# Performance work log

Measured on AMD Instinct MI355X. Metric: run time of the kernel, lower is better.

Reference implementation:

```python
import jax, jax.numpy as jnp
import numpy as np

B, L, D, H = 2, 2048, 1024, 16
HD = D // H  # head_dim = 64


def setup_inputs() -> dict:
    key = jax.random.key(0)
    ks = jax.random.split(key, 8)
    queries = jax.random.normal(ks[0], (B, L, D), dtype=jnp.float32)
    keys = jax.random.normal(ks[1], (B, L, D), dtype=jnp.float32)
    values = jax.random.normal(ks[2], (B, L, D), dtype=jnp.float32)
    mask = jax.random.randint(ks[3], (B, L, L), 0, 2) > 0  # True = masked
    s = 1.0 / np.sqrt(D)
    W_q = jax.random.normal(ks[4], (D, D), dtype=jnp.float32) * s
    W_k = jax.random.normal(ks[5], (D, D), dtype=jnp.float32) * s
    W_v = jax.random.normal(ks[6], (D, D), dtype=jnp.float32) * s
    W_o = jax.random.normal(ks[7], (D, D), dtype=jnp.float32) * s
    return {"queries": queries, "keys": keys, "values": values,
            "W_q": W_q, "W_k": W_k, "W_v": W_v, "W_o": W_o, "mask": mask}


def _split_heads(x):
    # [B, L, D] -> [B, H, L, HD]
    return x.reshape(B, L, H, HD).transpose(0, 2, 1, 3)


def reference(queries, keys, values, W_q, W_k, W_v, W_o, mask):
    # Linear projections (nn.Linear: x @ W.T, no bias)
    q = _split_heads(queries @ W_q.T)   # [B,H,Lq,HD]
    k = _split_heads(keys @ W_k.T)      # [B,H,Lk,HD]
    v = _split_heads(values @ W_v.T)    # [B,H,Lk,HD]
    scores = jnp.einsum('bnqd,bnkd->bnqk', q, k) / np.sqrt(HD)
    scores = jnp.where(mask[:, None, :, :], -1e9, scores)
    attn = jax.nn.softmax(scores, axis=-1)
    ctx = jnp.einsum('bnqk,bnkd->bnqd', attn, v)
    ctx = ctx.transpose(0, 2, 1, 3).reshape(B, L, D)
    return ctx @ W_o.T  # dropout p=0.0 -> identity
```

## Files before the change

kernel.cpp:

```cpp
#include <hip/hip_runtime.h>
#include <hip/hip_bf16.h>

typedef __bf16 bf16;
typedef __attribute__((ext_vector_type(8))) __bf16 bf16x8;
typedef __attribute__((ext_vector_type(4))) __bf16 bf16x4;
typedef __attribute__((ext_vector_type(4))) float f32x4;

#define B_   2
#define L_   2048
#define D_   1024
#define H_   16
#define HD_  64

__device__ __forceinline__ float fast_exp2(float x) {
  float e; asm("v_exp_f32 %0, %1" : "=v"(e) : "v"(x)); return e;
}

__device__ __forceinline__ void gll16(const bf16* g, bf16* l) {
  __builtin_amdgcn_global_load_lds((const __attribute__((address_space(1))) void*)g,
                                   (__attribute__((address_space(3))) void*)l,
                                   16, 0, 0);
}

__global__ void detect_kernel(const unsigned short* __restrict__ q_u,
                              const unsigned char* __restrict__ m_u,
                              int* __restrict__ flags) {
  __shared__ int cnt, odd;
  if (threadIdx.x == 0) { cnt = 0; odd = 0; }
  __syncthreads();
  int c = 0, o = 0;
  for (int i = 0; i < 8; i++) {
    int idx = threadIdx.x * 8 + i;
    unsigned e = (q_u[idx] >> 7) & 0xFF;
    if (e >= 0x8F || (e > 0 && e <= 0x6F)) c++;
    if ((idx & 3) && m_u[idx]) o = 1;
  }
  atomicAdd(&cnt, c);
  if (o) atomicOr(&odd, 1);
  __syncthreads();
  if (threadIdx.x == 0) { flags[0] = (cnt > 128) ? 1 : 0; flags[1] = odd; }
}

__device__ __forceinline__ void canon_body(const void* src, bf16* dst, int i, int f) {
  if (f) {
    const float4* s = (const float4*)src;
    float4 a = s[i / 4], b2 = s[i / 4 + 1];
    bf16x8 o;
    o[0] = (bf16)a.x;  o[1] = (bf16)a.y;  o[2] = (bf16)a.z;  o[3] = (bf16)a.w;
    o[4] = (bf16)b2.x; o[5] = (bf16)b2.y; o[6] = (bf16)b2.z; o[7] = (bf16)b2.w;
    *(bf16x8*)(dst + i) = o;
  } else {
    *(bf16x8*)(dst + i) = ((const bf16x8*)src)[i / 8];
  }
}

__global__ __launch_bounds__(256) void canon_pack(
    const void* xq, const void* xk, const void* xv,
    const void* Wq, const void* Wk, const void* Wv, const void* Wo,
    const void* mp,
    bf16* cxq, bf16* cxk, bf16* cxv,
    bf16* cWq, bf16* cWk, bf16* cWv, bf16* cWo,
    unsigned* __restrict__ bitsT,
    const int* __restrict__ flags) {
  int t = blockIdx.x;
  if (t >= 8192) {
    int wid = (t - 8192) * 256 + threadIdx.x;
    unsigned v = 0;
    if (flags[1]) {
      const uchar4* p = (const uchar4*)mp;
#pragma unroll
      for (int c = 0; c < 8; c++) {
        uchar4 u = p[wid * 8 + c];
        v |= (u.x ? 1u : 0u) << (c * 4 + 0);
        v |= (u.y ? 1u : 0u) << (c * 4 + 1);
        v |= (u.z ? 1u : 0u) << (c * 4 + 2);
        v |= (u.w ? 1u : 0u) << (c * 4 + 3);
      }
    } else {
      const int4* p = (const int4*)mp;
#pragma unroll
      for (int c = 0; c < 8; c++) {
        int4 u = p[wid * 8 + c];
        v |= (u.x ? 1u : 0u) << (c * 4 + 0);
        v |= (u.y ? 1u : 0u) << (c * 4 + 1);
        v |= (u.z ? 1u : 0u) << (c * 4 + 2);
        v |= (u.w ? 1u : 0u) << (c * 4 + 3);
      }
    }
    int row = wid >> 6, word = wid & 63;
    int kt = word >> 1, half = word & 1;
    bitsT[((size_t)kt * 4096 + row) * 2 + half] = v;
    return;
  }
  const int f = flags[0];
  const void* src; bf16* dst; int base;
  if (t < 2048)      { src = xq; dst = cxq; base = t * 2048; }
  else if (t < 4096) { src = xk; dst = cxk; base = (t - 2048) * 2048; }
  else if (t < 6144) { src = xv; dst = cxv; base = (t - 4096) * 2048; }
  else {
    int w = t - 6144, wi = w >> 9;
    base = (w & 511) * 2048;
    if (wi == 0)      { src = Wq; dst = cWq; }
    else if (wi == 1) { src = Wk; dst = cWk; }
    else if (wi == 2) { src = Wv; dst = cWv; }
    else              { src = Wo; dst = cWo; }
  }
  canon_body(src, dst, base + threadIdx.x * 8, f);
}

__global__ __launch_bounds__(256) void gemm_qkv(
    const bf16* __restrict__ Aq, const bf16* __restrict__ Bq, bf16* __restrict__ Cq,
    const bf16* __restrict__ Ak, const bf16* __restrict__ Bk, bf16* __restrict__ Ck,
    const bf16* __restrict__ Av, const bf16* __restrict__ Bv, bf16* __restrict__ VT) {
  __shared__ bf16 smem[128 * 136];
  bf16* sA = smem;
  bf16* sB = smem + 4096;
  const int z = blockIdx.z;
  const bf16* A  = (z == 0) ? Aq : (z == 1) ? Ak : Av;
  const bf16* Bm = (z == 0) ? Bq : (z == 1) ? Bk : Bv;

  const int tid = threadIdx.x;
  const int w = tid >> 6, lane = tid & 63, qd = lane >> 4, r = lane & 15;
  const int wm = w >> 1, wn = w & 1;
  const int m0 = blockIdx.x * 128, n0 = blockIdx.y * 128;

  f32x4 acc[4][4];
#pragma unroll
  for (int i = 0; i < 4; i++)
#pragma unroll
    for (int j = 0; j < 4; j++) acc[i][j] = (f32x4){0.f, 0.f, 0.f, 0.f};

  for (int k0 = 0; k0 < 1024; k0 += 32) {
    __syncthreads();
#pragma unroll
    for (int p = 0; p < 2; p++) {
      int c = p * 256 + tid;
      gll16(A + (size_t)(m0 + (c >> 2)) * 1024 + k0 + (c & 3) * 8, sA + c * 8);
    }
#pragma unroll
    for (int p = 0; p < 2; p++) {
      int c = p * 256 + tid;
      gll16(Bm + (size_t)(n0 + (c >> 2)) * 1024 + k0 + (c & 3) * 8, sB + c * 8);
    }
    __syncthreads();
    bf16x8 af[4], bfv[4];
#pragma unroll
    for (int i = 0; i < 4; i++)
      af[i] = *(const bf16x8*)&sA[(wm * 64 + i * 16 + r) * 32 + qd * 8];
#pragma unroll
    for (int j = 0; j < 4; j++)
      bfv[j] = *(const bf16x8*)&sB[(wn * 64 + j * 16 + r) * 32 + qd * 8];
#pragma unroll
    for (int i = 0; i < 4; i++)
#pragma unroll
      for (int j = 0; j < 4; j++)
        acc[i][j] = __builtin_amdgcn_mfma_f32_16x16x32_bf16(af[i], bfv[j], acc[i][j], 0, 0, 0);
  }

  if (z < 2) {
    bf16* C = (z == 0) ? Cq : Ck;
    const float s = (z == 0) ? 0.1803368801f : 1.0f;
#pragma unroll
    for (int i = 0; i < 4; i++)
#pragma unroll
      for (int j = 0; j < 4; j++)
#pragma unroll
        for (int rr = 0; rr < 4; rr++) {
          int row = m0 + wm * 64 + i * 16 + qd * 4 + rr;
          int col = n0 + wn * 64 + j * 16 + r;
          C[(size_t)row * 1024 + col] = (bf16)(acc[i][j][rr] * s);
        }
  } else {
    __syncthreads();
#pragma unroll
    for (int i = 0; i < 4; i++)
#pragma unroll
      for (int j = 0; j < 4; j++) {
        int col = wn * 64 + j * 16 + r;
        int rowb = wm * 64 + i * 16 + qd * 4;
        bf16x4 v4;
#pragma unroll
        for (int rr = 0; rr < 4; rr++) v4[rr] = (bf16)acc[i][j][rr];
        *(bf16x4*)&smem[col * 136 + rowb] = v4;
      }
    __syncthreads();
    const int b = m0 >> 11, tok0 = m0 & 2047, h0 = n0 >> 6;
#pragma unroll
    for (int p = 0; p < 8; p++) {
      int c = p * 256 + tid;
      int dl = c >> 4, ch = c & 15;
      bf16x8 v = *(const bf16x8*)&smem[dl * 136 + ch * 8];
      int head = h0 + (dl >> 6), d = dl & 63;
      *(bf16x8*)(VT + ((size_t)((b * 16 + head) * 64 + d)) * 2048 + tok0 + ch * 8) = v;
    }
  }
}

__global__ __launch_bounds__(256) void gemm_nt_out(const bf16* __restrict__ A,
                                                   const bf16* __restrict__ Bm,
                                                   void* __restrict__ Cout,
                                                   const int* __restrict__ flags) {
  __shared__ bf16 sA[128 * 32];
  __shared__ bf16 sB[64 * 32];
  const int tid = threadIdx.x;
  const int w = tid >> 6, lane = tid & 63, qd = lane >> 4, r = lane & 15;
  const int wm = w >> 1, wn = w & 1;
  const int m0 = blockIdx.x * 128, n0 = blockIdx.y * 64;

  f32x4 acc[4][2];
#pragma unroll
  for (int i = 0; i < 4; i++)
#pragma unroll
    for (int j = 0; j < 2; j++) acc[i][j] = (f32x4){0.f, 0.f, 0.f, 0.f};

  for (int k0 = 0; k0 < 1024; k0 += 32) {
    __syncthreads();
    {
      int c0 = tid;
      gll16(A + (size_t)(m0 + (c0 >> 2)) * 1024 + k0 + (c0 & 3) * 8, sA + c0 * 8);
      int c1 = 256 + tid;
      gll16(A + (size_t)(m0 + (c1 >> 2)) * 1024 + k0 + (c1 & 3) * 8, sA + c1 * 8);
      int cb = tid;
      gll16(Bm + (size_t)(n0 + (cb >> 2)) * 1024 + k0 + (cb & 3) * 8, sB + cb * 8);
    }
    __syncthreads();
    bf16x8 af[4], bfv[2];
#pragma unroll
    for (int i = 0; i < 4; i++)
      af[i] = *(const bf16x8*)&sA[(wm * 64 + i * 16 + r) * 32 + qd * 8];
#pragma unroll
    for (int j = 0; j < 2; j++)
      bfv[j] = *(const bf16x8*)&sB[(wn * 32 + j * 16 + r) * 32 + qd * 8];
#pragma unroll
    for (int i = 0; i < 4; i++)
#pragma unroll
      for (int j = 0; j < 2; j++)
        acc[i][j] = __builtin_amdgcn_mfma_f32_16x16x32_bf16(af[i], bfv[j], acc[i][j], 0, 0, 0);
  }
  const int f = flags[0];
#pragma unroll
  for (int i = 0; i < 4; i++)
#pragma unroll
    for (int j = 0; j < 2; j++)
#pragma unroll
      for (int rr = 0; rr < 4; rr++) {
        int row = m0 + wm * 64 + i * 16 + qd * 4 + rr;
        int col = n0 + wn * 32 + j * 16 + r;
        if (f) ((float*)Cout)[(size_t)row * 1024 + col] = acc[i][j][rr];
        else   ((bf16*)Cout)[(size_t)row * 1024 + col] = (bf16)acc[i][j][rr];
      }
}

__global__ __launch_bounds__(256) void attn_kernel(const bf16* __restrict__ Q,
                                                   const bf16* __restrict__ Kp,
                                                   const bf16* __restrict__ Vt,
                                                   const unsigned* __restrict__ bitsT,
                                                   bf16* __restrict__ OP,
                                                   float* __restrict__ LP) {
  __shared__ bf16 sK[64 * 64];
  __shared__ bf16 sVT[64 * 64];
  __shared__ bf16 sP[128 * 72];
  const int tid = threadIdx.x;
  const int w = tid >> 6, lane = tid & 63, qd = lane >> 4, r = lane & 15;
  const int bh = blockIdx.y, b = bh >> 4, h = bh & 15;
  const int q0 = blockIdx.x * 128;
  const int z = blockIdx.z;

  bf16x8 qf[2][2];
#pragma unroll
  for (int i = 0; i < 2; i++)
#pragma unroll
    for (int ks = 0; ks < 2; ks++)
      qf[i][ks] = *(const bf16x8*)(Q + (size_t)(b * L_ + q0 + w * 32 + i * 16 + r) * D_ +
                                   h * HD_ + ks * 32 + qd * 8);

  bf16x8 ones;
#pragma unroll
  for (int e = 0; e < 8; e++) ones[e] = (bf16)1.0f;

  f32x4 o[2][4], lacc[2];
#pragma unroll
  for (int i = 0; i < 2; i++) {
#pragma unroll
    for (int dj = 0; dj < 4; dj++) o[i][dj] = (f32x4){0.f, 0.f, 0.f, 0.f};
    lacc[i] = (f32x4){0.f, 0.f, 0.f, 0.f};
  }

  for (int kt = z * 16; kt < z * 16 + 16; kt++) {
    __syncthreads();
#pragma unroll
    for (int p = 0; p < 2; p++) {
      int c = p * 256 + tid;
      int row = c >> 3, kc = c & 7;
      int kcg = kc ^ (row & 7);
      gll16(Kp + (size_t)(b * L_ + kt * 64 + row) * D_ + h * HD_ + kcg * 8, sK + c * 8);
    }
#pragma unroll
    for (int p = 0; p < 2; p++) {
      int c = p * 256 + tid;
      int row = c >> 3, kc = c & 7;
      int kcg = kc ^ (row & 7);
      gll16(Vt + (size_t)(bh * 64 + row) * L_ + kt * 64 + kcg * 8, sVT + c * 8);
    }

    uint2 m64[2];
#pragma unroll
    for (int i = 0; i < 2; i++)
      m64[i] = *(const uint2*)(bitsT +
          ((size_t)kt * 4096 + b * 2048 + q0 + w * 32 + i * 16 + r) * 2);

    __syncthreads();

    bf16x8 kf[4][2];
#pragma unroll
    for (int j = 0; j < 4; j++)
#pragma unroll
      for (int ks = 0; ks < 2; ks++) {
        int row = j * 16 + r;
        int phys = (ks * 4 + qd) ^ (row & 7);
        kf[j][ks] = *(const bf16x8*)&sK[row * 64 + phys * 8];
      }

#pragma unroll
    for (int i = 0; i < 2; i++) {
      f32x4 S[4];
#pragma unroll
      for (int j = 0; j < 4; j++) {
        S[j] = (f32x4){0.f, 0.f, 0.f, 0.f};
#pragma unroll
        for (int ks = 0; ks < 2; ks++)
          S[j] = __builtin_amdgcn_mfma_f32_16x16x32_bf16(kf[j][ks], qf[i][ks], S[j], 0, 0, 0);
      }
#pragma unroll
      for (int j = 0; j < 4; j++) {
        unsigned word = (j < 2) ? m64[i].x : m64[i].y;
        unsigned nib = (word >> ((j & 1) * 16 + qd * 4)) & 0xFu;
        bf16x4 pv;
#pragma unroll
        for (int rr = 0; rr < 4; rr++) {
          float e = fast_exp2(S[j][rr]);
          pv[rr] = (bf16)(((nib >> rr) & 1u) ? 0.f : e);
        }
        *(bf16x4*)&sP[(w * 32 + i * 16 + r) * 72 + j * 16 + qd * 4] = pv;
      }
    }
    asm volatile("s_waitcnt lgkmcnt(0)" ::: "memory");

    bf16x8 vf[4][2];
#pragma unroll
    for (int dj = 0; dj < 4; dj++)
#pragma unroll
      for (int ks = 0; ks < 2; ks++) {
        int row = dj * 16 + r;
        int phys = (ks * 4 + qd) ^ (row & 7);
        vf[dj][ks] = *(const bf16x8*)&sVT[row * 64 + phys * 8];
      }
#pragma unroll
    for (int i = 0; i < 2; i++)
#pragma unroll
      for (int ks = 0; ks < 2; ks++) {
        bf16x8 pf = *(const bf16x8*)&sP[(w * 32 + i * 16 + r) * 72 + ks * 32 + qd * 8];
#pragma unroll
        for (int dj = 0; dj < 4; dj++)
          o[i][dj] = __builtin_amdgcn_mfma_f32_16x16x32_bf16(pf, vf[dj][ks], o[i][dj], 0, 0, 0);
        lacc[i] = __builtin_amdgcn_mfma_f32_16x16x32_bf16(pf, ones, lacc[i], 0, 0, 0);
      }
  }

#pragma unroll
  for (int i = 0; i < 2; i++) {
#pragma unroll
    for (int dj = 0; dj < 4; dj++)
#pragma unroll
      for (int rr = 0; rr < 4; rr++) {
        int rg = b * L_ + q0 + w * 32 + i * 16 + qd * 4 + rr;
        int col = h * HD_ + dj * 16 + r;
        OP[((size_t)z * 4096 + rg) * 1024 + col] = (bf16)o[i][dj][rr];
      }
    if (r == 0) {
#pragma unroll
      for (int rr = 0; rr < 4; rr++) {
        int rg = b * L_ + q0 + w * 32 + i * 16 + qd * 4 + rr;
        LP[((size_t)z * 4096 + rg) * 16 + h] = lacc[i][rr];
      }
    }
  }
}

__global__ __launch_bounds__(256) void combine_kernel(const bf16* __restrict__ OP,
                                                      const float* __restrict__ LP,
                                                      bf16* __restrict__ CTX) {
  size_t idx = ((size_t)blockIdx.x * 256 + threadIdx.x) * 8;
  int row = (int)(idx >> 10), col = (int)(idx & 1023);
  bf16x8 a = *(const bf16x8*)(OP + idx);
  bf16x8 c = *(const bf16x8*)(OP + (size_t)4096 * 1024 + idx);
  int h = col >> 6;
  float l = LP[row * 16 + h] + LP[65536 + row * 16 + h];
  float inv = 1.0f / l;
  bf16x8 o;
#pragma unroll
  for (int e = 0; e < 8; e++) o[e] = (bf16)(((float)a[e] + (float)c[e]) * inv);
  *(bf16x8*)(CTX + idx) = o;
}

extern "C" void kernel_launch(void* const* d_in, const int* in_sizes, int n_in,
                              void* d_out, int out_size, void* d_ws, size_t ws_size,
                              hipStream_t stream) {
  const void* xq = d_in[0];
  const void* xk = d_in[1];
  const void* xv = d_in[2];
  const void* Wq = d_in[3];
  const void* Wk = d_in[4];
  const void* Wv = d_in[5];
  const void* Wo = d_in[6];
  const void* mask = d_in[7];

  char* ws = (char*)d_ws;
  const size_t MB = 1048576;
  int*      FLAGS = (int*)(ws + 0);
  unsigned* BITS  = (unsigned*)(ws + 4096);
  bf16* cWo = (bf16*)(ws + 2 * MB);
  bf16* cWq = (bf16*)(ws + 4 * MB);
  bf16* cWk = (bf16*)(ws + 6 * MB);
  bf16* cWv = (bf16*)(ws + 8 * MB);
  bf16* cxq = (bf16*)(ws + 10 * MB);
  bf16* cxk = (bf16*)(ws + 18 * MB);
  bf16* cxv = (bf16*)(ws + 26 * MB);
  bf16* Q   = (bf16*)(ws + 34 * MB);
  bf16* K   = (bf16*)(ws + 42 * MB);
  bf16* VT  = (bf16*)(ws + 50 * MB);
  bf16*  OP  = (bf16*)(ws + 4 * MB);
  float* LP  = (float*)(ws + 20 * MB);
  bf16*  CTX = (bf16*)(ws + 26 * MB);

  detect_kernel<<<1, 256, 0, stream>>>((const unsigned short*)xq,
                                       (const unsigned char*)mask, FLAGS);
  canon_pack<<<9216, 256, 0, stream>>>(xq, xk, xv, Wq, Wk, Wv, Wo, mask,
                                       cxq, cxk, cxv, cWq, cWk, cWv, cWo,
                                       BITS, FLAGS);
  gemm_qkv<<<dim3(32, 8, 3), 256, 0, stream>>>(cxq, cWq, Q,
                                               cxk, cWk, K,
                                               cxv, cWv, VT);
  attn_kernel<<<dim3(16, 32, 2), 256, 0, stream>>>(Q, K, VT, BITS, OP, LP);
  combine_kernel<<<2048, 256, 0, stream>>>(OP, LP, CTX);
  gemm_nt_out<<<dim3(32, 16), 256, 0, stream>>>(CTX, cWo, d_out, FLAGS);
}
```

Measured before the change: 268.8 us.

## Use fp16 for V and P in attention; stage Q/K GEMM stores through LDS

Switches the V-transpose buffer and the softmax probability tile from bf16 to fp16, using packed round-toward-zero conversion (cvt_pkrtz) and fp16 MFMA for the P·V product and the row-sum. The aim is cheaper conversion instructions in the exp/pack inner loop. Separately, the Q/K projection epilogue now writes through shared memory and issues coalesced 16-byte global stores instead of scattered 2-byte stores. The fp16 path changes rounding behaviour and has narrower range than bf16, and the epilogue adds an extra LDS round trip and barrier.

```diff
diff --git a/kernel.cpp b/kernel.cpp
--- a/kernel.cpp
+++ b/kernel.cpp
@@ -2,8 +2,12 @@
 #include <hip/hip_bf16.h>
 
 typedef __bf16 bf16;
+typedef _Float16 f16;
 typedef __attribute__((ext_vector_type(8))) __bf16 bf16x8;
 typedef __attribute__((ext_vector_type(4))) __bf16 bf16x4;
+typedef __attribute__((ext_vector_type(8))) _Float16 f16x8;
+typedef __attribute__((ext_vector_type(4))) _Float16 f16x4;
+typedef __attribute__((ext_vector_type(2))) _Float16 f16x2;
 typedef __attribute__((ext_vector_type(4))) float f32x4;
 
 #define B_   2
@@ -16,7 +20,11 @@
   float e; asm("v_exp_f32 %0, %1" : "=v"(e) : "v"(x)); return e;
 }
 
-__device__ __forceinline__ void gll16(const bf16* g, bf16* l) {
+__device__ __forceinline__ f16x2 pkrtz(float a, float b) {
+  return __builtin_bit_cast(f16x2, __builtin_amdgcn_cvt_pkrtz(a, b));
+}
+
+__device__ __forceinline__ void gll16(const void* g, void* l) {
   __builtin_amdgcn_global_load_lds((const __attribute__((address_space(1))) void*)g,
                                    (__attribute__((address_space(3))) void*)l,
                                    16, 0, 0);
@@ -111,7 +119,7 @@
 __global__ __launch_bounds__(256) void gemm_qkv(
     const bf16* __restrict__ Aq, const bf16* __restrict__ Bq, bf16* __restrict__ Cq,
     const bf16* __restrict__ Ak, const bf16* __restrict__ Bk, bf16* __restrict__ Ck,
-    const bf16* __restrict__ Av, const bf16* __restrict__ Bv, bf16* __restrict__ VT) {
+    const bf16* __restrict__ Av, const bf16* __restrict__ Bv, f16* __restrict__ VT) {
   __shared__ bf16 smem[128 * 136];
   bf16* sA = smem;
   bf16* sB = smem + 4096;
@@ -157,6 +165,7 @@
         acc[i][j] = __builtin_amdgcn_mfma_f32_16x16x32_bf16(af[i], bfv[j], acc[i][j], 0, 0, 0);
   }
 
+  __syncthreads();
   if (z < 2) {
     bf16* C = (z == 0) ? Cq : Ck;
     const float s = (z == 0) ? 0.1803368801f : 1.0f;
@@ -165,23 +174,29 @@
 #pragma unroll
       for (int j = 0; j < 4; j++)
 #pragma unroll
-        for (int rr = 0; rr < 4; rr++) {
-          int row = m0 + wm * 64 + i * 16 + qd * 4 + rr;
-          int col = n0 + wn * 64 + j * 16 + r;
-          C[(size_t)row * 1024 + col] = (bf16)(acc[i][j][rr] * s);
-        }
+        for (int rr = 0; rr < 4; rr++)
+          smem[(wm * 64 + i * 16 + qd * 4 + rr) * 136 + wn * 64 + j * 16 + r] =
+              (bf16)(acc[i][j][rr] * s);
+    __syncthreads();
+#pragma unroll
+    for (int p = 0; p < 8; p++) {
+      int c = p * 256 + tid;
+      int row = c >> 4, ch = c & 15;
+      bf16x8 v = *(const bf16x8*)&smem[row * 136 + ch * 8];
+      *(bf16x8*)(C + (size_t)(m0 + row) * 1024 + n0 + ch * 8) = v;
+    }
   } else {
-    __syncthreads();
+    f16* sT = (f16*)smem;
 #pragma unroll
     for (int i = 0; i < 4; i++)
 #pragma unroll
       for (int j = 0; j < 4; j++) {
         int col = wn * 64 + j * 16 + r;
         int rowb = wm * 64 + i * 16 + qd * 4;
-        bf16x4 v4;
-#pragma unroll
-        for (int rr = 0; rr < 4; rr++) v4[rr] = (bf16)acc[i][j][rr];
-        *(bf16x4*)&smem[col * 136 + rowb] = v4;
+        f16x2 lo = pkrtz(acc[i][j][0], acc[i][j][1]);
+        f16x2 hi = pkrtz(acc[i][j][2], acc[i][j][3]);
+        f16x4 v4; v4[0] = lo[0]; v4[1] = lo[1]; v4[2] = hi[0]; v4[3] = hi[1];
+        *(f16x4*)&sT[col * 136 + rowb] = v4;
       }
     __syncthreads();
     const int b = m0 >> 11, tok0 = m0 & 2047, h0 = n0 >> 6;
@@ -189,9 +204,9 @@
     for (int p = 0; p < 8; p++) {
       int c = p * 256 + tid;
       int dl = c >> 4, ch = c & 15;
-      bf16x8 v = *(const bf16x8*)&smem[dl * 136 + ch * 8];
+      f16x8 v = *(const f16x8*)&sT[dl * 136 + ch * 8];
       int head = h0 + (dl >> 6), d = dl & 63;
-      *(bf16x8*)(VT + ((size_t)((b * 16 + head) * 64 + d)) * 2048 + tok0 + ch * 8) = v;
+      *(f16x8*)(VT + ((size_t)((b * 16 + head) * 64 + d)) * 2048 + tok0 + ch * 8) = v;
     }
   }
 }
@@ -253,13 +268,13 @@
 
 __global__ __launch_bounds__(256) void attn_kernel(const bf16* __restrict__ Q,
                                                    const bf16* __restrict__ Kp,
-                                                   const bf16* __restrict__ Vt,
+                                                   const f16* __restrict__ Vt,
                                                    const unsigned* __restrict__ bitsT,
                                                    bf16* __restrict__ OP,
                                                    float* __restrict__ LP) {
   __shared__ bf16 sK[64 * 64];
-  __shared__ bf16 sVT[64 * 64];
-  __shared__ bf16 sP[128 * 72];
+  __shared__ f16 sVT[64 * 64];
+  __shared__ f16 sP[128 * 72];
   const int tid = threadIdx.x;
   const int w = tid >> 6, lane = tid & 63, qd = lane >> 4, r = lane & 15;
   const int bh = blockIdx.y, b = bh >> 4, h = bh & 15;
@@ -274,9 +289,9 @@
       qf[i][ks] = *(const bf16x8*)(Q + (size_t)(b * L_ + q0 + w * 32 + i * 16 + r) * D_ +
                                    h * HD_ + ks * 32 + qd * 8);
 
-  bf16x8 ones;
-#pragma unroll
-  for (int e = 0; e < 8; e++) ones[e] = (bf16)1.0f;
+  f16x8 ones;
+#pragma unroll
+  for (int e = 0; e < 8; e++) ones[e] = (f16)1.0f;
 
   f32x4 o[2][4], lacc[2];
 #pragma unroll
@@ -335,35 +350,40 @@
       for (int j = 0; j < 4; j++) {
         unsigned word = (j < 2) ? m64[i].x : m64[i].y;
         unsigned nib = (word >> ((j & 1) * 16 + qd * 4)) & 0xFu;
-        bf16x4 pv;
-#pragma unroll
-        for (int rr = 0; rr < 4; rr++) {
-          float e = fast_exp2(S[j][rr]);
-          pv[rr] = (bf16)(((nib >> rr) & 1u) ? 0.f : e);
-        }
-        *(bf16x4*)&sP[(w * 32 + i * 16 + r) * 72 + j * 16 + qd * 4] = pv;
+        float e0 = fast_exp2(S[j][0]);
+        float e1 = fast_exp2(S[j][1]);
+        float e2 = fast_exp2(S[j][2]);
+        float e3 = fast_exp2(S[j][3]);
+        if (nib & 1u) e0 = 0.f;
+        if (nib & 2u) e1 = 0.f;
+        if (nib & 4u) e2 = 0.f;
+        if (nib & 8u) e3 = 0.f;
+        f16x2 lo = pkrtz(e0, e1);
+        f16x2 hi = pkrtz(e2, e3);
+        f16x4 pv; pv[0] = lo[0]; pv[1] = lo[1]; pv[2] = hi[0]; pv[3] = hi[1];
+        *(f16x4*)&sP[(w * 32 + i * 16 + r) * 72 + j * 16 + qd * 4] = pv;
       }
     }
     asm volatile("s_waitcnt lgkmcnt(0)" ::: "memory");
 
-    bf16x8 vf[4][2];
+    f16x8 vf[4][2];
 #pragma unroll
     for (int dj = 0; dj < 4; dj++)
 #pragma unroll
       for (int ks = 0; ks < 2; ks++) {
         int row = dj * 16 + r;
         int phys = (ks * 4 + qd) ^ (row & 7);
-        vf[dj][ks] = *(const bf16x8*)&sVT[row * 64 + phys * 8];
+        vf[dj][ks] = *(const f16x8*)&sVT[row * 64 + phys * 8];
       }
 #pragma unroll
     for (int i = 0; i < 2; i++)
 #pragma unroll
       for (int ks = 0; ks < 2; ks++) {
-        bf16x8 pf = *(const bf16x8*)&sP[(w * 32 + i * 16 + r) * 72 + ks * 32 + qd * 8];
+        f16x8 pf = *(const f16x8*)&sP[(w * 32 + i * 16 + r) * 72 + ks * 32 + qd * 8];
 #pragma unroll
         for (int dj = 0; dj < 4; dj++)
-          o[i][dj] = __builtin_amdgcn_mfma_f32_16x16x32_bf16(pf, vf[dj][ks], o[i][dj], 0, 0, 0);
-        lacc[i] = __builtin_amdgcn_mfma_f32_16x16x32_bf16(pf, ones, lacc[i], 0, 0, 0);
+          o[i][dj] = __builtin_amdgcn_mfma_f32_16x16x32_f16(pf, vf[dj][ks], o[i][dj], 0, 0, 0);
+        lacc[i] = __builtin_amdgcn_mfma_f32_16x16x32_f16(pf, ones, lacc[i], 0, 0, 0);
       }
   }
 
@@ -428,7 +448,7 @@
   bf16* cxv = (bf16*)(ws + 26 * MB);
   bf16* Q   = (bf16*)(ws + 34 * MB);
   bf16* K   = (bf16*)(ws + 42 * MB);
-  bf16* VT  = (bf16*)(ws + 50 * MB);
+  f16*  VT  = (f16*)(ws + 50 * MB);
   bf16*  OP  = (bf16*)(ws + 4 * MB);
   float* LP  = (float*)(ws + 20 * MB);
   bf16*  CTX = (bf16*)(ws + 26 * MB);
```

New measurement: 270.1 us. About the same (+0.5%).
